# Kernel tuning notes

Measured on AMD Instinct MI355X. Metric: run time of the kernel, lower is better.

## Reference

```python
import jax, jax.numpy as jnp
import numpy as np

NEG = -1e9


def _layer_norm(x, g, b, eps=1e-5):
    m = x.mean(-1, keepdims=True)
    v = x.var(-1, keepdims=True)
    return (x - m) / jnp.sqrt(v + eps) * g + b


def _gat(x, mask, W, a):
    # x: [B,N,Fin], W: [Fin,Fout], a: [2*Fout]
    h = x @ W                                   # [B,N,Fout]
    F = W.shape[1]
    src = h @ a[:F]                             # [B,N]
    dst = h @ a[F:]                             # [B,N]
    e = jax.nn.leaky_relu(src[:, :, None] + dst[:, None, :], 0.2)  # [B,N,N]
    e = jnp.where(mask, e, NEG)
    attn = jax.nn.softmax(e, axis=-1)
    return attn @ h, attn


def _mha(x, mask, Wq, bq, Wk, bk, Wv, bv, Wo, bo, num_heads, head_dim):
    B, N, _ = x.shape
    q = (x @ Wq + bq).reshape(B, N, num_heads, head_dim)
    k = (x @ Wk + bk).reshape(B, N, num_heads, head_dim)
    v = (x @ Wv + bv).reshape(B, N, num_heads, head_dim)
    scores = jnp.einsum('bihd,bjhd->bhij', q, k) / jnp.sqrt(jnp.asarray(head_dim, x.dtype))
    scores = jnp.where(mask[:, None, :, :], scores, NEG)
    attn = jax.nn.softmax(scores, axis=-1)      # [B,H,N,N]
    ctx = jnp.einsum('bhij,bjhd->bihd', attn, v).reshape(B, N, num_heads * head_dim)
    return ctx @ Wo + bo, attn


def setup_inputs() -> dict:
    key = jax.random.key(0)
    ks = jax.random.split(key, 32)
    B, N = 64, 400
    D, Hd, E, H = 400, 256, 128, 4
    hd = Hd // H  # 64
    s = 0.02
    x = jax.random.normal(ks[0], (B, N, D), dtype=jnp.float32)
    adj = (jax.random.uniform(ks[1], (B, N, N)) < 0.15).astype(jnp.float32)
    eye = jnp.eye(N, dtype=jnp.float32)
    adj = jnp.maximum(adj, eye[None])
    def w(k, shape):
        return jax.random.normal(k, shape, dtype=jnp.float32) * s
    return {
        'x': x, 'adj': adj,
        'Wq': w(ks[2], (D, H * hd)), 'bq': jnp.zeros(H * hd),
        'Wk': w(ks[3], (D, H * hd)), 'bk': jnp.zeros(H * hd),
        'Wv': w(ks[4], (D, H * hd)), 'bv': jnp.zeros(H * hd),
        'Wo': w(ks[5], (H * hd, D)), 'bo': jnp.zeros(D),
        'gat1_W': w(ks[6], (D, Hd)), 'gat1_a': w(ks[7], (2 * Hd,)),
        'gat2_W': w(ks[8], (Hd, Hd)), 'gat2_a': w(ks[9], (2 * Hd,)),
        'gat3_W': w(ks[10], (Hd, E)), 'gat3_a': w(ks[11], (2 * E,)),
        'res1_W': w(ks[12], (D, Hd)), 'res1_b': jnp.zeros(Hd),
        'res2_W': w(ks[13], (Hd, Hd)), 'res2_b': jnp.zeros(Hd),
        'res3_W': w(ks[14], (Hd, E)), 'res3_b': jnp.zeros(E),
        'ln1_g': jnp.ones(Hd), 'ln1_b': jnp.zeros(Hd),
        'ln2_g': jnp.ones(Hd), 'ln2_b': jnp.zeros(Hd),
        'ln3_g': jnp.ones(E), 'ln3_b': jnp.zeros(E),
    }


def reference(x, adj, Wq, bq, Wk, bk, Wv, bv, Wo, bo,
              gat1_W, gat1_a, gat2_W, gat2_a, gat3_W, gat3_a,
              res1_W, res1_b, res2_W, res2_b, res3_W, res3_b,
              ln1_g, ln1_b, ln2_g, ln2_b, ln3_g, ln3_b):
    mask = adj > 0
    # eval mode: dropout is identity
    mha_out, _ = _mha(x, mask, Wq, bq, Wk, bk, Wv, bv, Wo, bo, num_heads=4, head_dim=64)
    x = x + mha_out
    g1, attn1 = _gat(x, mask, gat1_W, gat1_a)
    x = jax.nn.elu(_layer_norm(g1 + (x @ res1_W + res1_b), ln1_g, ln1_b))
    g2, attn2 = _gat(x, mask, gat2_W, gat2_a)
    x = jax.nn.elu(_layer_norm(g2 + (x @ res2_W + res2_b), ln2_g, ln2_b))
    g3, attn3 = _gat(x, mask, gat3_W, gat3_a)
    x = _layer_norm(g3 + (x @ res3_W + res3_b), ln3_g, ln3_b)
    return x, (attn1, attn2, attn3)
```

## Files before the change

### kernel.cpp

```cpp
#include <hip/hip_runtime.h>


#define NEGBIG (-1e9f)

typedef __attribute__((ext_vector_type(8))) short bf16x8;
typedef __attribute__((ext_vector_type(4))) float f32x4;

__device__ inline unsigned short f2bf(float f) {
    unsigned u = __builtin_bit_cast(unsigned, f);
    u += 0x7fffu + ((u >> 16) & 1u);
    return (unsigned short)(u >> 16);
}
__device__ inline float bf2f(unsigned short h) {
    unsigned u = ((unsigned)h) << 16;
    return __builtin_bit_cast(float, u);
}

__device__ inline float wave_sum(float v) {
#pragma unroll
    for (int off = 32; off >= 1; off >>= 1)
        v += __shfl_xor(v, off, 64);
    return v;
}
__device__ inline float wave_max(float v) {
#pragma unroll
    for (int off = 32; off >= 1; off >>= 1)
        v = fmaxf(v, __shfl_xor(v, off, 64));
    return v;
}

__global__ void build_biases(
    float* bqkv, const float* bq, const float* bk, const float* bv,
    float* bgr1, const float* r1b, float* bgr2, const float* r2b,
    float* bgr3, const float* r3b)
{
    const int t = threadIdx.x;
    bqkv[t] = bq[t]; bqkv[256 + t] = bk[t]; bqkv[512 + t] = bv[t];
    bgr1[t] = 0.f; bgr1[256 + t] = r1b[t];
    bgr2[t] = 0.f; bgr2[256 + t] = r2b[t];
    if (t < 128) { bgr3[t] = 0.f; bgr3[128 + t] = r3b[t]; }
}

__global__ __launch_bounds__(256) void adj2mask(
    const float* __restrict__ adj, unsigned short* __restrict__ mb)
{
    const long i = ((long)blockIdx.x * 256 + threadIdx.x) * 4;
    const float4 a = *reinterpret_cast<const float4*>(adj + i);
    ushort4 o;
    o.x = f2bf(a.x > 0.f ? 0.f : NEGBIG);
    o.y = f2bf(a.y > 0.f ? 0.f : NEGBIG);
    o.z = f2bf(a.z > 0.f ? 0.f : NEGBIG);
    o.w = f2bf(a.w > 0.f ? 0.f : NEGBIG);
    *reinterpret_cast<ushort4*>(mb + i) = o;
}

__global__ __launch_bounds__(256) void transpose_to_bf16(
    const float* __restrict__ in, unsigned short* __restrict__ out,
    int R, int C, int ldIn, long sIn, long sOut)
{
    in  += (long)blockIdx.z * sIn;
    out += (long)blockIdx.z * sOut;
    __shared__ float t[32][33];
    const int r0 = blockIdx.y * 32, c0 = blockIdx.x * 32;
    const int tid = threadIdx.x;

    const int row = tid >> 3, c4 = tid & 7;
    float4 v = make_float4(0.f, 0.f, 0.f, 0.f);
    if (r0 + row < R && c0 + c4 * 4 < C)
        v = *reinterpret_cast<const float4*>(&in[(long)(r0 + row) * ldIn + c0 + c4 * 4]);
    t[row][c4 * 4 + 0] = v.x;
    t[row][c4 * 4 + 1] = v.y;
    t[row][c4 * 4 + 2] = v.z;
    t[row][c4 * 4 + 3] = v.w;
    __syncthreads();

    const int oc = tid >> 3, r4 = tid & 7;
    if (c0 + oc < C && r0 + r4 * 4 < R) {
        ushort4 o;
        o.x = f2bf(t[r4 * 4 + 0][oc]);
        o.y = f2bf(t[r4 * 4 + 1][oc]);
        o.z = f2bf(t[r4 * 4 + 2][oc]);
        o.w = f2bf(t[r4 * 4 + 3][oc]);
        *reinterpret_cast<ushort4*>(&out[(long)(c0 + oc) * R + r0 + r4 * 4]) = o;
    }
}

template<bool BIAS, bool ACCUM, bool RESID, bool ABHALF, bool OUTBF16>
__global__ __launch_bounds__(512) void gemm_mfma(
    const void* __restrict__ Av, const unsigned short* __restrict__ BT,
    const float* __restrict__ bias, const float* __restrict__ resid,
    void* __restrict__ Cv, int M, int K, int Nc, int ldA, int ldC,
    long sA, long sBT, long sC)
{
    const int bz = blockIdx.z;
    const float* Af = ABHALF ? nullptr : ((const float*)Av + (long)bz * sA);
    const unsigned short* Ah = ABHALF ? ((const unsigned short*)Av + (long)bz * sA) : nullptr;
    BT += (long)bz * sBT;
    float* Cf = OUTBF16 ? nullptr : ((float*)Cv + (long)bz * sC);
    unsigned short* Ch = OUTBF16 ? ((unsigned short*)Cv + (long)bz * sC) : nullptr;
    const float* Rp = RESID ? (resid + (long)bz * sC) : nullptr;

    __shared__ short As[128][40];
    __shared__ short Bs[256][40];

    const int tid = threadIdx.x;
    const int lane = tid & 63, wave = tid >> 6;
    const int wm = wave >> 2, wn = wave & 3;
    const int m0 = blockIdx.y * 128, n0 = blockIdx.x * 256;

    f32x4 acc[4][4] = {};

    const int nk = (K + 31) / 32;
    for (int kt = 0; kt < nk; ++kt) {
        const int k0 = kt * 32;
        __syncthreads();
        if (ABHALF) {
            const int row = tid >> 2, k8 = tid & 3;
            const int gm = m0 + row, gk = k0 + k8 * 8;
            uint4 av = make_uint4(0u, 0u, 0u, 0u);
            if (gm < M && gk < K)
                av = *reinterpret_cast<const uint4*>(&Ah[(long)gm * ldA + gk]);
            *reinterpret_cast<uint4*>(&As[row][k8 * 8]) = av;
        } else {
#pragma unroll
            for (int p = 0; p < 2; ++p) {
                const int idx = tid + p * 512;
                const int row = idx >> 3, k4 = idx & 7;
                const int gm = m0 + row, gk = k0 + k4 * 4;
                float4 av = make_float4(0.f, 0.f, 0.f, 0.f);
                if (gm < M && gk < K)
                    av = *reinterpret_cast<const float4*>(&Af[(long)gm * ldA + gk]);
                ushort4 h4;
                h4.x = f2bf(av.x); h4.y = f2bf(av.y); h4.z = f2bf(av.z); h4.w = f2bf(av.w);
                *reinterpret_cast<ushort4*>(&As[row][k4 * 4]) = h4;
            }
        }
#pragma unroll
        for (int p = 0; p < 2; ++p) {
            const int idx = tid + p * 512;
            const int n = idx >> 2, k8 = idx & 3;
            const int gn = n0 + n, gk = k0 + k8 * 8;
            uint4 bv = make_uint4(0u, 0u, 0u, 0u);
            if (gn < Nc && gk < K)
                bv = *reinterpret_cast<const uint4*>(&BT[(long)gn * K + gk]);
            *reinterpret_cast<uint4*>(&Bs[n][k8 * 8]) = bv;
        }
        __syncthreads();

        const int fr = lane & 15, fkb = (lane >> 4) * 8;
        bf16x8 a[4], b[4];
#pragma unroll
        for (int i = 0; i < 4; ++i)
            a[i] = *reinterpret_cast<const bf16x8*>(&As[wm * 64 + i * 16 + fr][fkb]);
#pragma unroll
        for (int j = 0; j < 4; ++j)
            b[j] = *reinterpret_cast<const bf16x8*>(&Bs[wn * 64 + j * 16 + fr][fkb]);
#pragma unroll
        for (int i = 0; i < 4; ++i)
#pragma unroll
            for (int j = 0; j < 4; ++j)
                acc[i][j] = __builtin_amdgcn_mfma_f32_16x16x32_bf16(a[i], b[j], acc[i][j], 0, 0, 0);
    }

    const int fr = lane & 15, rg = lane >> 4;
#pragma unroll
    for (int i = 0; i < 4; ++i) {
#pragma unroll
        for (int j = 0; j < 4; ++j) {
#pragma unroll
            for (int r = 0; r < 4; ++r) {
                const int gm = m0 + wm * 64 + i * 16 + rg * 4 + r;
                const int gn = n0 + wn * 64 + j * 16 + fr;
                if (gm < M && gn < Nc) {
                    float v = acc[i][j][r];
                    if (BIAS)  v += bias[gn];
                    if (RESID) v += Rp[(long)gm * ldC + gn];
                    if (OUTBF16) {
                        Ch[(long)gm * ldC + gn] = f2bf(v);
                    } else {
                        if (ACCUM) v += Cf[(long)gm * ldC + gn];
                        Cf[(long)gm * ldC + gn] = v;
                    }
                }
            }
        }
    }
}

__global__ __launch_bounds__(256) void mha_flash_mfma(
    const unsigned short* __restrict__ qkv, const unsigned short* __restrict__ mask,
    unsigned short* __restrict__ ctx, int ld)
{
    const int it = blockIdx.x, h = blockIdx.y, b = blockIdx.z;
    const int i0 = it * 64;
    const int tid = threadIdx.x;
    const int lane = tid & 63, w = tid >> 6;
    const int c = lane & 15, g = lane >> 4;
    const unsigned short NEGBF = f2bf(NEGBIG);

    __shared__ short Qs[64][72];
    __shared__ short Ks[64][72];
    __shared__ short Vt[64][72];
    __shared__ short Ps[64][72];
    __shared__ short Adjs[64][72];

    const long base_q = ((long)b * 400 + i0) * ld + h * 64;
#pragma unroll
    for (int p = 0; p < 2; ++p) {
        const int idx = tid + p * 256;
        const int r = idx >> 3, c8 = idx & 7;
        uint4 qv = make_uint4(0u, 0u, 0u, 0u);
        if (i0 + r < 400)
            qv = *reinterpret_cast<const uint4*>(qkv + base_q + (long)r * ld + c8 * 8);
        *reinterpret_cast<uint4*>(&Qs[r][c8 * 8]) = qv;
    }

    f32x4 o[4] = {};
    float m[4] = {-3e38f, -3e38f, -3e38f, -3e38f};
    float l[4] = {0.f, 0.f, 0.f, 0.f};

    for (int jt = 0; jt < 7; ++jt) {
        const int j0 = jt * 64;
        __syncthreads();

        const long base_k = ((long)b * 400 + j0) * ld + 256 + h * 64;
        const long base_v = base_k + 256;
#pragma unroll
        for (int p = 0; p < 2; ++p) {
            const int idx = tid + p * 256;
            const int r = idx >> 3, c8 = idx & 7;
            uint4 kv = make_uint4(0u, 0u, 0u, 0u);
            if (j0 + r < 400)
                kv = *reinterpret_cast<const uint4*>(qkv + base_k + (long)r * ld + c8 * 8);
            *reinterpret_cast<uint4*>(&Ks[r][c8 * 8]) = kv;

            ushort4 mb = make_ushort4(NEGBF, NEGBF, NEGBF, NEGBF);
            ushort4 mb2 = mb;
            if (i0 + r < 400 && j0 + c8 * 8 + 7 < 400) {
                const uint4 mv = *reinterpret_cast<const uint4*>(
                    mask + ((long)b * 400 + i0 + r) * 400 + j0 + c8 * 8);
                mb  = *reinterpret_cast<const ushort4*>(&mv.x);
                mb2 = *reinterpret_cast<const ushort4*>(&mv.z);
            }
            *reinterpret_cast<ushort4*>(&Adjs[r][c8 * 8]) = mb;
            *reinterpret_cast<ushort4*>(&Adjs[r][c8 * 8 + 4]) = mb2;
        }
        {
            const int j4 = tid >> 4, d4 = tid & 15;
            ushort4 vl[4];
#pragma unroll
            for (int t = 0; t < 4; ++t) {
                vl[t] = make_ushort4(0, 0, 0, 0);
                if (j0 + j4 * 4 + t < 400)
                    vl[t] = *reinterpret_cast<const ushort4*>(qkv + base_v + (long)(j4 * 4 + t) * ld + d4 * 4);
            }
#pragma unroll
            for (int u = 0; u < 4; ++u) {
                ushort4 h4;
                h4.x = ((const unsigned short*)&vl[0])[u];
                h4.y = ((const unsigned short*)&vl[1])[u];
                h4.z = ((const unsigned short*)&vl[2])[u];
                h4.w = ((const unsigned short*)&vl[3])[u];
                *reinterpret_cast<ushort4*>(&Vt[d4 * 4 + u][j4 * 4]) = h4;
            }
        }
        __syncthreads();

        f32x4 s4[4] = {};
#pragma unroll
        for (int ks = 0; ks < 2; ++ks) {
            const bf16x8 a = *reinterpret_cast<const bf16x8*>(&Qs[w * 16 + c][ks * 32 + g * 8]);
#pragma unroll
            for (int t = 0; t < 4; ++t) {
                const bf16x8 bb = *reinterpret_cast<const bf16x8*>(&Ks[t * 16 + c][ks * 32 + g * 8]);
                s4[t] = __builtin_amdgcn_mfma_f32_16x16x32_bf16(a, bb, s4[t], 0, 0, 0);
            }
        }

        float e[4][4];
        float pmax[4];
#pragma unroll
        for (int reg = 0; reg < 4; ++reg) {
            const int qr = w * 16 + g * 4 + reg;
            float mx = -3e38f;
#pragma unroll
            for (int t = 0; t < 4; ++t) {
                const float ev = s4[t][reg] * 0.125f + bf2f((unsigned short)Adjs[qr][t * 16 + c]);
                e[t][reg] = ev;
                mx = fmaxf(mx, ev);
            }
            pmax[reg] = mx;
        }
#pragma unroll
        for (int reg = 0; reg < 4; ++reg)
#pragma unroll
            for (int off = 1; off <= 8; off <<= 1)
                pmax[reg] = fmaxf(pmax[reg], __shfl_xor(pmax[reg], off, 64));

        float al[4];
#pragma unroll
        for (int reg = 0; reg < 4; ++reg) {
            const float mn = fmaxf(m[reg], pmax[reg]);
            al[reg] = __expf(m[reg] - mn);
            m[reg] = mn;
        }

#pragma unroll
        for (int reg = 0; reg < 4; ++reg) {
            const int qr = w * 16 + g * 4 + reg;
            float psum = 0.f;
#pragma unroll
            for (int t = 0; t < 4; ++t) {
                const float p = __expf(e[t][reg] - m[reg]);
                psum += p;
                Ps[qr][t * 16 + c] = (short)f2bf(p);
            }
            l[reg] = l[reg] * al[reg] + psum;
        }

#pragma unroll
        for (int dt = 0; dt < 4; ++dt)
#pragma unroll
            for (int reg = 0; reg < 4; ++reg)
                o[dt][reg] *= al[reg];

#pragma unroll
        for (int ks = 0; ks < 2; ++ks) {
            const bf16x8 a = *reinterpret_cast<const bf16x8*>(&Ps[w * 16 + c][ks * 32 + g * 8]);
#pragma unroll
            for (int dt = 0; dt < 4; ++dt) {
                const bf16x8 bb = *reinterpret_cast<const bf16x8*>(&Vt[dt * 16 + c][ks * 32 + g * 8]);
                o[dt] = __builtin_amdgcn_mfma_f32_16x16x32_bf16(a, bb, o[dt], 0, 0, 0);
            }
        }
    }

#pragma unroll
    for (int reg = 0; reg < 4; ++reg)
#pragma unroll
        for (int off = 1; off <= 8; off <<= 1)
            l[reg] += __shfl_xor(l[reg], off, 64);

#pragma unroll
    for (int reg = 0; reg < 4; ++reg) {
        const int gi = i0 + w * 16 + g * 4 + reg;
        if (gi < 400) {
            const float inv = 1.f / l[reg];
#pragma unroll
            for (int dt = 0; dt < 4; ++dt)
                ctx[((long)b * 400 + gi) * 256 + h * 64 + dt * 16 + c] = f2bf(o[dt][reg] * inv);
        }
    }
}

__global__ __launch_bounds__(256) void gat_srcdst(
    const float* __restrict__ h, const float* __restrict__ a,
    float* __restrict__ src, float* __restrict__ dst, int F, int ld)
{
    const int row = blockIdx.x * 4 + (threadIdx.x >> 6);
    const int lane = threadIdx.x & 63;
    const float* hp = h + (long)row * ld;
    float s = 0.f, d = 0.f;
    for (int f = lane; f < F; f += 64) {
        const float hv = hp[f];
        s += hv * a[f];
        d += hv * a[F + f];
    }
    s = wave_sum(s);
    d = wave_sum(d);
    if (lane == 0) { src[row] = s; dst[row] = d; }
}

__global__ __launch_bounds__(256) void gat_attn(
    const float* __restrict__ src, const float* __restrict__ dst,
    const unsigned short* __restrict__ mask,
    float* __restrict__ attn, unsigned short* __restrict__ attnb)
{
    const int row = blockIdx.x * 4 + (threadIdx.x >> 6);
    const int b = row / 400;
    const int lane = threadIdx.x & 63;
    const float si = src[row];
    const float* db = dst + (long)b * 400;
    const unsigned short* mrow = mask + (long)row * 400;

    float e[7];
    float mx = -3.0e38f;
#pragma unroll
    for (int t = 0; t < 7; ++t) {
        const int j = lane + 64 * t;
        float v = -3.0e38f;
        if (j < 400) {
            v = si + db[j];
            v = (v > 0.f) ? v : 0.2f * v;
            v += bf2f(mrow[j]);
        }
        e[t] = v;
        mx = fmaxf(mx, v);
    }
    mx = wave_max(mx);

    float p[7];
    float sum = 0.f;
#pragma unroll
    for (int t = 0; t < 7; ++t) {
        const int j = lane + 64 * t;
        if (j < 400) {
            p[t] = __expf(e[t] - mx);
            sum += p[t];
        }
    }
    sum = wave_sum(sum);
    const float inv = 1.f / sum;
#pragma unroll
    for (int t = 0; t < 7; ++t) {
        const int j = lane + 64 * t;
        if (j < 400) {
            const float pv = p[t] * inv;
            attn[(long)row * 400 + j] = pv;
            attnb[(long)row * 400 + j] = f2bf(pv);
        }
    }
}

template<int F, bool ELU, bool OB16>
__global__ __launch_bounds__(256) void ln_kernel(
    const float* __restrict__ in, int ldIn, const float* __restrict__ g,
    const float* __restrict__ b, void* __restrict__ outv)
{
    const int row = blockIdx.x * 4 + (threadIdx.x >> 6);
    const int lane = threadIdx.x & 63;
    constexpr int PER = F / 64;
    const float* ip = in + (long)row * ldIn;

    float v[PER];
    float s = 0.f;
#pragma unroll
    for (int t = 0; t < PER; ++t) {
        v[t] = ip[lane + 64 * t];
        s += v[t];
    }
    s = wave_sum(s);
    const float mean = s * (1.f / F);
    float vs = 0.f;
#pragma unroll
    for (int t = 0; t < PER; ++t) {
        const float d = v[t] - mean;
        vs += d * d;
    }
    vs = wave_sum(vs);
    const float rstd = rsqrtf(vs * (1.f / F) + 1e-5f);
#pragma unroll
    for (int t = 0; t < PER; ++t) {
        const int col = lane + 64 * t;
        float y = (v[t] - mean) * rstd * g[col] + b[col];
        if (ELU) y = (y > 0.f) ? y : expm1f(y);
        if (OB16) ((unsigned short*)outv)[(long)row * F + col] = f2bf(y);
        else      ((float*)outv)[(long)row * F + col] = y;
    }
}

extern "C" void kernel_launch(void* const* d_in, const int* in_sizes, int n_in,
                              void* d_out, int out_size, void* d_ws, size_t ws_size,
                              hipStream_t stream) {
    const float* x    = (const float*)d_in[0];
    const float* adj  = (const float*)d_in[1];
    const float* Wq   = (const float*)d_in[2];
    const float* bq   = (const float*)d_in[3];
    const float* Wk   = (const float*)d_in[4];
    const float* bk   = (const float*)d_in[5];
    const float* Wv   = (const float*)d_in[6];
    const float* bv   = (const float*)d_in[7];
    const float* Wo   = (const float*)d_in[8];
    const float* bo   = (const float*)d_in[9];
    const float* g1W  = (const float*)d_in[10];
    const float* g1a  = (const float*)d_in[11];
    const float* g2W  = (const float*)d_in[12];
    const float* g2a  = (const float*)d_in[13];
    const float* g3W  = (const float*)d_in[14];
    const float* g3a  = (const float*)d_in[15];
    const float* r1W  = (const float*)d_in[16];
    const float* r1b  = (const float*)d_in[17];
    const float* r2W  = (const float*)d_in[18];
    const float* r2b  = (const float*)d_in[19];
    const float* r3W  = (const float*)d_in[20];
    const float* r3b  = (const float*)d_in[21];
    const float* ln1g = (const float*)d_in[22];
    const float* ln1b = (const float*)d_in[23];
    const float* ln2g = (const float*)d_in[24];
    const float* ln2b = (const float*)d_in[25];
    const float* ln3g = (const float*)d_in[26];
    const float* ln3b = (const float*)d_in[27];

    float* out_x = (float*)d_out;
    float* attn1 = out_x + 3276800;
    float* attn2 = attn1 + 10240000;
    float* attn3 = attn2 + 10240000;

    char* wsb = (char*)d_ws;
    float*          hrF  = (float*)wsb;
    unsigned short* ctxH = (unsigned short*)wsb;
    unsigned short* qkvH  = (unsigned short*)(wsb + 52428800);
    unsigned short* attnH = qkvH;
    unsigned short* x2H   = qkvH;
    unsigned short* hT    = (unsigned short*)(wsb + 72908800);
    unsigned short* maskH = (unsigned short*)(wsb + 91750400);
    float* srcb = (float*)(wsb + 112230400);
    float* dstb = (float*)(wsb + 112332800);
    unsigned short* wT = (unsigned short*)(wsb + 112435200);
    unsigned short* wTq  = wT;
    unsigned short* wTk  = wT + 102400;
    unsigned short* wTv  = wT + 204800;
    unsigned short* wTo  = wT + 307200;
    unsigned short* wTg1 = wT + 409600;
    unsigned short* wTr1 = wT + 512000;
    unsigned short* wTg2 = wT + 614400;
    unsigned short* wTr2 = wT + 679936;
    unsigned short* wTg3 = wT + 745472;
    unsigned short* wTr3 = wT + 778240;
    float* bqkv = (float*)(wsb + 114057216);
    float* bgr1 = bqkv + 768;
    float* bgr2 = bgr1 + 512;
    float* bgr3 = bgr2 + 512;
    unsigned short* xcH = (unsigned short*)attn1;

    const dim3 b256(256), b512(512);
    const int M = 25600;

    build_biases<<<1, b256, 0, stream>>>(bqkv, bq, bk, bv, bgr1, r1b, bgr2, r2b, bgr3, r3b);
    adj2mask<<<dim3(10000), b256, 0, stream>>>(adj, maskH);
    transpose_to_bf16<<<dim3(8, 13), b256, 0, stream>>>(Wq,  wTq, 400, 256, 256, 0, 0);
    transpose_to_bf16<<<dim3(8, 13), b256, 0, stream>>>(Wk,  wTk, 400, 256, 256, 0, 0);
    transpose_to_bf16<<<dim3(8, 13), b256, 0, stream>>>(Wv,  wTv, 400, 256, 256, 0, 0);
    transpose_to_bf16<<<dim3(13, 8), b256, 0, stream>>>(Wo,  wTo, 256, 400, 400, 0, 0);
    transpose_to_bf16<<<dim3(8, 13), b256, 0, stream>>>(g1W, wTg1, 400, 256, 256, 0, 0);
    transpose_to_bf16<<<dim3(8, 13), b256, 0, stream>>>(r1W, wTr1, 400, 256, 256, 0, 0);
    transpose_to_bf16<<<dim3(8, 8),  b256, 0, stream>>>(g2W, wTg2, 256, 256, 256, 0, 0);
    transpose_to_bf16<<<dim3(8, 8),  b256, 0, stream>>>(r2W, wTr2, 256, 256, 256, 0, 0);
    transpose_to_bf16<<<dim3(4, 8),  b256, 0, stream>>>(g3W, wTg3, 256, 128, 128, 0, 0);
    transpose_to_bf16<<<dim3(4, 8),  b256, 0, stream>>>(r3W, wTr3, 256, 128, 128, 0, 0);

    gemm_mfma<true, false, false, false, true><<<dim3(3, 200), b512, 0, stream>>>(
        x, wTq, bqkv, nullptr, qkvH, M, 400, 768, 400, 768, 0, 0, 0);
    mha_flash_mfma<<<dim3(7, 4, 64), b256, 0, stream>>>(qkvH, maskH, ctxH, 768);
    gemm_mfma<true, false, true, true, true><<<dim3(2, 200), b512, 0, stream>>>(
        ctxH, wTo, bo, x, xcH, M, 256, 400, 256, 400, 0, 0, 0);

    gemm_mfma<true, false, false, true, false><<<dim3(2, 200), b512, 0, stream>>>(
        xcH, wTg1, bgr1, nullptr, hrF, M, 400, 512, 400, 512, 0, 0, 0);
    gat_srcdst<<<dim3(6400), b256, 0, stream>>>(hrF, g1a, srcb, dstb, 256, 512);
    gat_attn<<<dim3(6400), b256, 0, stream>>>(srcb, dstb, maskH, attn1, attnH);
    transpose_to_bf16<<<dim3(8, 13, 64), b256, 0, stream>>>(hrF, hT, 400, 256, 512, 204800, 102400);
    gemm_mfma<false, true, false, true, false><<<dim3(1, 4, 64), b512, 0, stream>>>(
        attnH, hT, nullptr, nullptr, hrF + 256, 400, 400, 256, 400, 512, 160000, 102400, 204800);
    ln_kernel<256, true, true><<<dim3(6400), b256, 0, stream>>>(hrF + 256, 512, ln1g, ln1b, x2H);

    gemm_mfma<true, false, false, true, false><<<dim3(2, 200), b512, 0, stream>>>(
        x2H, wTg2, bgr2, nullptr, hrF, M, 256, 512, 256, 512, 0, 0, 0);
    gat_srcdst<<<dim3(6400), b256, 0, stream>>>(hrF, g2a, srcb, dstb, 256, 512);
    gat_attn<<<dim3(6400), b256, 0, stream>>>(srcb, dstb, maskH, attn2, attnH);
    transpose_to_bf16<<<dim3(8, 13, 64), b256, 0, stream>>>(hrF, hT, 400, 256, 512, 204800, 102400);
    gemm_mfma<false, true, false, true, false><<<dim3(1, 4, 64), b512, 0, stream>>>(
        attnH, hT, nullptr, nullptr, hrF + 256, 400, 400, 256, 400, 512, 160000, 102400, 204800);
    ln_kernel<256, true, true><<<dim3(6400), b256, 0, stream>>>(hrF + 256, 512, ln2g, ln2b, x2H);

    gemm_mfma<true, false, false, true, false><<<dim3(1, 200), b512, 0, stream>>>(
        x2H, wTg3, bgr3, nullptr, hrF, M, 256, 256, 256, 256, 0, 0, 0);
    gat_srcdst<<<dim3(6400), b256, 0, stream>>>(hrF, g3a, srcb, dstb, 128, 256);
    gat_attn<<<dim3(6400), b256, 0, stream>>>(srcb, dstb, maskH, attn3, attnH);
    transpose_to_bf16<<<dim3(4, 13, 64), b256, 0, stream>>>(hrF, hT, 400, 128, 256, 102400, 51200);
    gemm_mfma<false, true, false, true, false><<<dim3(1, 4, 64), b512, 0, stream>>>(
        attnH, hT, nullptr, nullptr, hrF + 128, 400, 400, 128, 400, 256, 160000, 51200, 102400);
    ln_kernel<128, false, false><<<dim3(6400), b256, 0, stream>>>(hrF + 128, 256, ln3g, ln3b, out_x);
}
```

Measured before the change: 760.6 us.

## Fuse GAT softmax, attention-matmul, residual and layernorm into one kernel with bf16 h

Each GAT layer now has a single fused kernel. It computes the masked softmax rows into shared memory, writes the fp32 attention output, multiplies by h with MFMA while transposing h on the fly, then adds the residual and applies LayerNorm/ELU. The GEMM producing h and the residual now writes bf16, and src/dst are read from bf16. This drops the bf16 attention round trip, the per-batch transpose kernel, the separate LN kernel and the fp32 h traffic. The cost is lower precision in h and the residual, and a fused kernel with only 448 blocks and a large shared-memory footprint, which may limit occupancy.

After: 710.5 us. 1.07x faster.

```diff
diff --git a/kernel.cpp b/kernel.cpp
--- a/kernel.cpp
+++ b/kernel.cpp
@@ -56,10 +56,8 @@
 
 __global__ __launch_bounds__(256) void transpose_to_bf16(
     const float* __restrict__ in, unsigned short* __restrict__ out,
-    int R, int C, int ldIn, long sIn, long sOut)
+    int R, int C, int ldIn)
 {
-    in  += (long)blockIdx.z * sIn;
-    out += (long)blockIdx.z * sOut;
     __shared__ float t[32][33];
     const int r0 = blockIdx.y * 32, c0 = blockIdx.x * 32;
     const int tid = threadIdx.x;
@@ -85,20 +83,16 @@
     }
 }
 
-template<bool BIAS, bool ACCUM, bool RESID, bool ABHALF, bool OUTBF16>
+template<bool BIAS, bool RESID, bool ABHALF, bool OUTBF16>
 __global__ __launch_bounds__(512) void gemm_mfma(
     const void* __restrict__ Av, const unsigned short* __restrict__ BT,
     const float* __restrict__ bias, const float* __restrict__ resid,
-    void* __restrict__ Cv, int M, int K, int Nc, int ldA, int ldC,
-    long sA, long sBT, long sC)
+    void* __restrict__ Cv, int M, int K, int Nc, int ldA, int ldC)
 {
-    const int bz = blockIdx.z;
-    const float* Af = ABHALF ? nullptr : ((const float*)Av + (long)bz * sA);
-    const unsigned short* Ah = ABHALF ? ((const unsigned short*)Av + (long)bz * sA) : nullptr;
-    BT += (long)bz * sBT;
-    float* Cf = OUTBF16 ? nullptr : ((float*)Cv + (long)bz * sC);
-    unsigned short* Ch = OUTBF16 ? ((unsigned short*)Cv + (long)bz * sC) : nullptr;
-    const float* Rp = RESID ? (resid + (long)bz * sC) : nullptr;
+    const float* Af = ABHALF ? nullptr : (const float*)Av;
+    const unsigned short* Ah = ABHALF ? (const unsigned short*)Av : nullptr;
+    float* Cf = OUTBF16 ? nullptr : (float*)Cv;
+    unsigned short* Ch = OUTBF16 ? (unsigned short*)Cv : nullptr;
 
     __shared__ short As[128][40];
     __shared__ short Bs[256][40];
@@ -174,13 +168,9 @@
                 if (gm < M && gn < Nc) {
                     float v = acc[i][j][r];
                     if (BIAS)  v += bias[gn];
-                    if (RESID) v += Rp[(long)gm * ldC + gn];
-                    if (OUTBF16) {
-                        Ch[(long)gm * ldC + gn] = f2bf(v);
-                    } else {
-                        if (ACCUM) v += Cf[(long)gm * ldC + gn];
-                        Cf[(long)gm * ldC + gn] = v;
-                    }
+                    if (RESID) v += resid[(long)gm * ldC + gn];
+                    if (OUTBF16) Ch[(long)gm * ldC + gn] = f2bf(v);
+                    else         Cf[(long)gm * ldC + gn] = v;
                 }
             }
         }
@@ -353,109 +343,166 @@
     }
 }
 
-__global__ __launch_bounds__(256) void gat_srcdst(
-    const float* __restrict__ h, const float* __restrict__ a,
-    float* __restrict__ src, float* __restrict__ dst, int F, int ld)
-{
-    const int row = blockIdx.x * 4 + (threadIdx.x >> 6);
-    const int lane = threadIdx.x & 63;
-    const float* hp = h + (long)row * ld;
-    float s = 0.f, d = 0.f;
-    for (int f = lane; f < F; f += 64) {
-        const float hv = hp[f];
-        s += hv * a[f];
-        d += hv * a[F + f];
-    }
-    s = wave_sum(s);
-    d = wave_sum(d);
-    if (lane == 0) { src[row] = s; dst[row] = d; }
-}
-
-__global__ __launch_bounds__(256) void gat_attn(
-    const float* __restrict__ src, const float* __restrict__ dst,
-    const unsigned short* __restrict__ mask,
-    float* __restrict__ attn, unsigned short* __restrict__ attnb)
-{
-    const int row = blockIdx.x * 4 + (threadIdx.x >> 6);
-    const int b = row / 400;
-    const int lane = threadIdx.x & 63;
-    const float si = src[row];
-    const float* db = dst + (long)b * 400;
-    const unsigned short* mrow = mask + (long)row * 400;
-
-    float e[7];
-    float mx = -3.0e38f;
-#pragma unroll
-    for (int t = 0; t < 7; ++t) {
-        const int j = lane + 64 * t;
-        float v = -3.0e38f;
-        if (j < 400) {
-            v = si + db[j];
-            v = (v > 0.f) ? v : 0.2f * v;
-            v += bf2f(mrow[j]);
-        }
-        e[t] = v;
-        mx = fmaxf(mx, v);
-    }
-    mx = wave_max(mx);
-
-    float p[7];
-    float sum = 0.f;
-#pragma unroll
-    for (int t = 0; t < 7; ++t) {
-        const int j = lane + 64 * t;
-        if (j < 400) {
-            p[t] = __expf(e[t] - mx);
-            sum += p[t];
-        }
-    }
-    sum = wave_sum(sum);
-    const float inv = 1.f / sum;
-#pragma unroll
-    for (int t = 0; t < 7; ++t) {
-        const int j = lane + 64 * t;
-        if (j < 400) {
-            const float pv = p[t] * inv;
-            attn[(long)row * 400 + j] = pv;
-            attnb[(long)row * 400 + j] = f2bf(pv);
-        }
-    }
-}
-
-template<int F, bool ELU, bool OB16>
-__global__ __launch_bounds__(256) void ln_kernel(
-    const float* __restrict__ in, int ldIn, const float* __restrict__ g,
-    const float* __restrict__ b, void* __restrict__ outv)
+template<int F>
+__global__ __launch_bounds__(256) void gat_srcdst_h(
+    const unsigned short* __restrict__ h, const float* __restrict__ a,
+    float* __restrict__ src, float* __restrict__ dst)
 {
     const int row = blockIdx.x * 4 + (threadIdx.x >> 6);
     const int lane = threadIdx.x & 63;
     constexpr int PER = F / 64;
-    const float* ip = in + (long)row * ldIn;
-
-    float v[PER];
-    float s = 0.f;
-#pragma unroll
-    for (int t = 0; t < PER; ++t) {
-        v[t] = ip[lane + 64 * t];
-        s += v[t];
+    const unsigned short* hp = h + (long)row * (2 * F) + lane * PER;
+    float s = 0.f, d = 0.f;
+#pragma unroll
+    for (int u = 0; u < PER; ++u) {
+        const float hv = bf2f(hp[u]);
+        s += hv * a[lane * PER + u];
+        d += hv * a[F + lane * PER + u];
     }
     s = wave_sum(s);
-    const float mean = s * (1.f / F);
-    float vs = 0.f;
-#pragma unroll
-    for (int t = 0; t < PER; ++t) {
-        const float d = v[t] - mean;
-        vs += d * d;
-    }
-    vs = wave_sum(vs);
-    const float rstd = rsqrtf(vs * (1.f / F) + 1e-5f);
-#pragma unroll
-    for (int t = 0; t < PER; ++t) {
-        const int col = lane + 64 * t;
-        float y = (v[t] - mean) * rstd * g[col] + b[col];
-        if (ELU) y = (y > 0.f) ? y : expm1f(y);
-        if (OB16) ((unsigned short*)outv)[(long)row * F + col] = f2bf(y);
-        else      ((float*)outv)[(long)row * F + col] = y;
+    d = wave_sum(d);
+    if (lane == 0) { src[row] = s; dst[row] = d; }
+}
+
+template<int F, bool ELU, bool OUTB16>
+__global__ __launch_bounds__(256) void gat_fused(
+    const float* __restrict__ src, const float* __restrict__ dst,
+    const unsigned short* __restrict__ mask,
+    const unsigned short* __restrict__ hr,
+    const float* __restrict__ gam, const float* __restrict__ bet,
+    float* __restrict__ attn, void* __restrict__ xout)
+{
+    constexpr int LD = 2 * F;
+    constexpr int DT = F / 16;
+    constexpr int DG = F / 4;
+    constexpr int NP = (8 * DG) / 256;
+
+    const int it = blockIdx.x, b = blockIdx.y;
+    const int i0 = it * 64;
+    const int tid = threadIdx.x;
+    const int lane = tid & 63, w = tid >> 6;
+    const int c = lane & 15, g = lane >> 4;
+
+    __shared__ short Ps[64][424];
+    __shared__ short Ht[F][40];
+
+    const float* drow = dst + (long)b * 400;
+    for (int rr = 0; rr < 16; ++rr) {
+        const int r = w * 16 + rr;
+        const int gi = i0 + r;
+        const int giq = gi < 400 ? gi : 399;
+        const float si = src[(long)b * 400 + giq];
+        const unsigned short* mrow = mask + ((long)b * 400 + giq) * 400;
+        float e[7];
+        float mx = -3e38f;
+#pragma unroll
+        for (int t = 0; t < 7; ++t) {
+            const int j = lane + 64 * t;
+            float v = -3e38f;
+            if (j < 400) {
+                v = si + drow[j];
+                v = (v > 0.f) ? v : 0.2f * v;
+                v += bf2f(mrow[j]);
+            }
+            e[t] = v;
+            mx = fmaxf(mx, v);
+        }
+        mx = wave_max(mx);
+        float p[7], sum = 0.f;
+#pragma unroll
+        for (int t = 0; t < 7; ++t) {
+            const int j = lane + 64 * t;
+            if (j < 400) { p[t] = __expf(e[t] - mx); sum += p[t]; }
+        }
+        sum = wave_sum(sum);
+        const float inv = 1.f / sum;
+#pragma unroll
+        for (int t = 0; t < 7; ++t) {
+            const int j = lane + 64 * t;
+            if (j < 400) {
+                const float pv = p[t] * inv;
+                if (gi < 400) attn[((long)b * 400 + gi) * 400 + j] = pv;
+                Ps[r][j] = (short)f2bf(pv);
+            } else if (j < 416) {
+                Ps[r][j] = 0;
+            }
+        }
+    }
+
+    f32x4 acc[DT] = {};
+    const long hbase = (long)b * 400 * LD;
+    for (int kt = 0; kt < 13; ++kt) {
+        const int k0 = kt * 32;
+        __syncthreads();
+#pragma unroll
+        for (int p = 0; p < NP; ++p) {
+            const int slot = tid + p * 256;
+            const int kg = slot / DG, dg = slot % DG;
+            ushort4 vl[4];
+#pragma unroll
+            for (int t = 0; t < 4; ++t) {
+                const int j = k0 + kg * 4 + t;
+                vl[t] = make_ushort4(0, 0, 0, 0);
+                if (j < 400)
+                    vl[t] = *reinterpret_cast<const ushort4*>(&hr[hbase + (long)j * LD + dg * 4]);
+            }
+#pragma unroll
+            for (int u = 0; u < 4; ++u) {
+                ushort4 h4;
+                h4.x = ((const unsigned short*)&vl[0])[u];
+                h4.y = ((const unsigned short*)&vl[1])[u];
+                h4.z = ((const unsigned short*)&vl[2])[u];
+                h4.w = ((const unsigned short*)&vl[3])[u];
+                *reinterpret_cast<ushort4*>(&Ht[dg * 4 + u][kg * 4]) = h4;
+            }
+        }
+        __syncthreads();
+
+        const bf16x8 a = *reinterpret_cast<const bf16x8*>(&Ps[w * 16 + c][k0 + g * 8]);
+#pragma unroll
+        for (int dt = 0; dt < DT; ++dt) {
+            const bf16x8 bb = *reinterpret_cast<const bf16x8*>(&Ht[dt * 16 + c][g * 8]);
+            acc[dt] = __builtin_amdgcn_mfma_f32_16x16x32_bf16(a, bb, acc[dt], 0, 0, 0);
+        }
+    }
+
+#pragma unroll
+    for (int reg = 0; reg < 4; ++reg) {
+        const int row = w * 16 + g * 4 + reg;
+        const int gi = i0 + row;
+        const int giq = gi < 400 ? gi : 399;
+        const long rb = hbase + (long)giq * LD + F;
+        float v[DT];
+        float s = 0.f;
+#pragma unroll
+        for (int dt = 0; dt < DT; ++dt) {
+            v[dt] = acc[dt][reg] + bf2f(hr[rb + dt * 16 + c]);
+            s += v[dt];
+        }
+#pragma unroll
+        for (int off = 1; off <= 8; off <<= 1) s += __shfl_xor(s, off, 64);
+        const float mean = s * (1.f / F);
+        float vs = 0.f;
+#pragma unroll
+        for (int dt = 0; dt < DT; ++dt) {
+            const float d = v[dt] - mean;
+            vs += d * d;
+        }
+#pragma unroll
+        for (int off = 1; off <= 8; off <<= 1) vs += __shfl_xor(vs, off, 64);
+        const float rstd = rsqrtf(vs * (1.f / F) + 1e-5f);
+        if (gi < 400) {
+#pragma unroll
+            for (int dt = 0; dt < DT; ++dt) {
+                const int col = dt * 16 + c;
+                float y = (v[dt] - mean) * rstd * gam[col] + bet[col];
+                if (ELU) y = (y > 0.f) ? y : expm1f(y);
+                if (OUTB16)
+                    ((unsigned short*)xout)[((long)b * 400 + gi) * F + col] = f2bf(y);
+                else
+                    ((float*)xout)[((long)b * 400 + gi) * F + col] = y;
+            }
+        }
     }
 }
 
@@ -497,12 +544,10 @@
     float* attn3 = attn2 + 10240000;
 
     char* wsb = (char*)d_ws;
-    float*          hrF  = (float*)wsb;
+    unsigned short* hrH  = (unsigned short*)wsb;
     unsigned short* ctxH = (unsigned short*)wsb;
-    unsigned short* qkvH  = (unsigned short*)(wsb + 52428800);
-    unsigned short* attnH = qkvH;
-    unsigned short* x2H   = qkvH;
-    unsigned short* hT    = (unsigned short*)(wsb + 72908800);
+    unsigned short* qkvH = (unsigned short*)(wsb + 52428800);
+    unsigned short* x2H  = qkvH;
     unsigned short* maskH = (unsigned short*)(wsb + 91750400);
     float* srcb = (float*)(wsb + 112230400);
     float* dstb = (float*)(wsb + 112332800);
@@ -528,47 +573,38 @@
 
     build_biases<<<1, b256, 0, stream>>>(bqkv, bq, bk, bv, bgr1, r1b, bgr2, r2b, bgr3, r3b);
     adj2mask<<<dim3(10000), b256, 0, stream>>>(adj, maskH);
-    transpose_to_bf16<<<dim3(8, 13), b256, 0, stream>>>(Wq,  wTq, 400, 256, 256, 0, 0);
-    transpose_to_bf16<<<dim3(8, 13), b256, 0, stream>>>(Wk,  wTk, 400, 256, 256, 0, 0);
-    transpose_to_bf16<<<dim3(8, 13), b256, 0, stream>>>(Wv,  wTv, 400, 256, 256, 0, 0);
-    transpose_to_bf16<<<dim3(13, 8), b256, 0, stream>>>(Wo,  wTo, 256, 400, 400, 0, 0);
-    transpose_to_bf16<<<dim3(8, 13), b256, 0, stream>>>(g1W, wTg1, 400, 256, 256, 0, 0);
-    transpose_to_bf16<<<dim3(8, 13), b256, 0, stream>>>(r1W, wTr1, 400, 256, 256, 0, 0);
-    transpose_to_bf16<<<dim3(8, 8),  b256, 0, stream>>>(g2W, wTg2, 256, 256, 256, 0, 0);
-    transpose_to_bf16<<<dim3(8, 8),  b256, 0, stream>>>(r2W, wTr2, 256, 256, 256, 0, 0);
-    transpose_to_bf16<<<dim3(4, 8),  b256, 0, stream>>>(g3W, wTg3, 256, 128, 128, 0, 0);
-    transpose_to_bf16<<<dim3(4, 8),  b256, 0, stream>>>(r3W, wTr3, 256, 128, 128, 0, 0);
-
-    gemm_mfma<true, false, false, false, true><<<dim3(3, 200), b512, 0, stream>>>(
-        x, wTq, bqkv, nullptr, qkvH, M, 400, 768, 400, 768, 0, 0, 0);
+    transpose_to_bf16<<<dim3(8, 13), b256, 0, stream>>>(Wq,  wTq, 400, 256, 256);
+    transpose_to_bf16<<<dim3(8, 13), b256, 0, stream>>>(Wk,  wTk, 400, 256, 256);
+    transpose_to_bf16<<<dim3(8, 13), b256, 0, stream>>>(Wv,  wTv, 400, 256, 256);
+    transpose_to_bf16<<<dim3(13, 8), b256, 0, stream>>>(Wo,  wTo, 256, 400, 400);
+    transpose_to_bf16<<<dim3(8, 13), b256, 0, stream>>>(g1W, wTg1, 400, 256, 256);
+    transpose_to_bf16<<<dim3(8, 13), b256, 0, stream>>>(r1W, wTr1, 400, 256, 256);
+    transpose_to_bf16<<<dim3(8, 8),  b256, 0, stream>>>(g2W, wTg2, 256, 256, 256);
+    transpose_to_bf16<<<dim3(8, 8),  b256, 0, stream>>>(r2W, wTr2, 256, 256, 256);
+    transpose_to_bf16<<<dim3(4, 8),  b256, 0, stream>>>(g3W, wTg3, 256, 128, 128);
+    transpose_to_bf16<<<dim3(4, 8),  b256, 0, stream>>>(r3W, wTr3, 256, 128, 128);
+
+    gemm_mfma<true, false, false, true><<<dim3(3, 200), b512, 0, stream>>>(
+        x, wTq, bqkv, nullptr, qkvH, M, 400, 768, 400, 768);
     mha_flash_mfma<<<dim3(7, 4, 64), b256, 0, stream>>>(qkvH, maskH, ctxH, 768);
-    gemm_mfma<true, false, true, true, true><<<dim3(2, 200), b512, 0, stream>>>(
-        ctxH, wTo, bo, x, xcH, M, 256, 400, 256, 400, 0, 0, 0);
-
-    gemm_mfma<true, false, false, true, false><<<dim3(2, 200), b512, 0, stream>>>(
-        xcH, wTg1, bgr1, nullptr, hrF, M, 400, 512, 400, 512, 0, 0, 0);
-    gat_srcdst<<<dim3(6400), b256, 0, stream>>>(hrF, g1a, srcb, dstb, 256, 512);
-    gat_attn<<<dim3(6400), b256, 0, stream>>>(srcb, dstb, maskH, attn1, attnH);
-    transpose_to_bf16<<<dim3(8, 13, 64), b256, 0, stream>>>(hrF, hT, 400, 256, 512, 204800, 102400);
-    gemm_mfma<false, true, false, true, false><<<dim3(1, 4, 64), b512, 0, stream>>>(
-        attnH, hT, nullptr, nullptr, hrF + 256, 400, 400, 256, 400, 512, 160000, 102400, 204800);
-    ln_kernel<256, true, true><<<dim3(6400), b256, 0, stream>>>(hrF + 256, 512, ln1g, ln1b, x2H);
-
-    gemm_mfma<true, false, false, true, false><<<dim3(2, 200), b512, 0, stream>>>(
-        x2H, wTg2, bgr2, nullptr, hrF, M, 256, 512, 256, 512, 0, 0, 0);
-    gat_srcdst<<<dim3(6400), b256, 0, stream>>>(hrF, g2a, srcb, dstb, 256, 512);
-    gat_attn<<<dim3(6400), b256, 0, stream>>>(srcb, dstb, maskH, attn2, attnH);
-    transpose_to_bf16<<<dim3(8, 13, 64), b256, 0, stream>>>(hrF, hT, 400, 256, 512, 204800, 102400);
-    gemm_mfma<false, true, false, true, false><<<dim3(1, 4, 64), b512, 0, stream>>>(
-        attnH, hT, nullptr, nullptr, hrF + 256, 400, 400, 256, 400, 512, 160000, 102400, 204800);
-    ln_kernel<256, true, true><<<dim3(6400), b256, 0, stream>>>(hrF + 256, 512, ln2g, ln2b, x2H);
-
-    gemm_mfma<true, false, false, true, false><<<dim3(1, 200), b512, 0, stream>>>(
-        x2H, wTg3, bgr3, nullptr, hrF, M, 256, 256, 256, 256, 0, 0, 0);
-    gat_srcdst<<<dim3(6400), b256, 0, stream>>>(hrF, g3a, srcb, dstb, 128, 256);
-    gat_attn<<<dim3(6400), b256, 0, stream>>>(srcb, dstb, maskH, attn3, attnH);
-    transpose_to_bf16<<<dim3(4, 13, 64), b256, 0, stream>>>(hrF, hT, 400, 128, 256, 102400, 51200);
-    gemm_mfma<false, true, false, true, false><<<dim3(1, 4, 64), b512, 0, stream>>>(
-        attnH, hT, nullptr, nullptr, hrF + 128, 400, 400, 128, 400, 256, 160000, 51200, 102400);
-    ln_kernel<128, false, false><<<dim3(6400), b256, 0, stream>>>(hrF + 128, 256, ln3g, ln3b, out_x);
-}
+    gemm_mfma<true, true, true, true><<<dim3(2, 200), b512, 0, stream>>>(
+        ctxH, wTo, bo, x, xcH, M, 256, 400, 256, 400);
+
+    gemm_mfma<true, false, true, true><<<dim3(2, 200), b512, 0, stream>>>(
+        xcH, wTg1, bgr1, nullptr, hrH, M, 400, 512, 400, 512);
+    gat_srcdst_h<256><<<dim3(6400), b256, 0, stream>>>(hrH, g1a, srcb, dstb);
+    gat_fused<256, true, true><<<dim3(7, 64), b256, 0, stream>>>(
+        srcb, dstb, maskH, hrH, ln1g, ln1b, attn1, x2H);
+
+    gemm_mfma<true, false, true, true><<<dim3(2, 200), b512, 0, stream>>>(
+        x2H, wTg2, bgr2, nullptr, hrH, M, 256, 512, 256, 512);
+    gat_srcdst_h<256><<<dim3(6400), b256, 0, stream>>>(hrH, g2a, srcb, dstb);
+    gat_fused<256, true, true><<<dim3(7, 64), b256, 0, stream>>>(
+        srcb, dstb, maskH, hrH, ln2g, ln2b, attn2, x2H);
+
+    gemm_mfma<true, false, true, true><<<dim3(1, 200), b512, 0, stream>>>(
+        x2H, wTg3, bgr3, nullptr, hrH, M, 256, 256, 256, 256);
+    gat_srcdst_h<128><<<dim3(6400), b256, 0, stream>>>(hrH, g3a, srcb, dstb);
+    gat_fused<128, false, false><<<dim3(7, 64), b256, 0, stream>>>(
+        srcb, dstb, maskH, hrH, ln3g, ln3b, attn3, out_x);
+}
```
